# Kernel tuning notes

Measured on AMD Instinct MI355X. Metric: run time of the kernel, lower is better.

Reference implementation:

```python
import jax, jax.numpy as jnp
import numpy as np

VOCAB, EMB, H, NL = 50257, 1024, 2048, 2


def _lstm_cell(x, h, c, Wih, Whh, bih, bhh):
    # x: [1, in], h/c: [1, H]; PyTorch gate order i, f, g, o
    gates = x @ Wih.T + bih + h @ Whh.T + bhh  # [1, 4H]
    i, f, g, o = jnp.split(gates, 4, axis=-1)
    c2 = jax.nn.sigmoid(f) * c + jax.nn.sigmoid(i) * jnp.tanh(g)
    h2 = jax.nn.sigmoid(o) * jnp.tanh(c2)
    return h2, c2


def setup_inputs() -> dict:
    key = jax.random.key(0)
    ks = jax.random.split(key, 12)
    s = 0.02  # keep gate pre-activations in a sane range
    return {
        "input_ids": jax.random.randint(ks[0], (1,), 0, VOCAB, dtype=jnp.int64),
        "h0": jax.random.normal(ks[1], (2 * NL, 1, H), jnp.float32) * 0.1,
        "c0": jax.random.normal(ks[2], (2 * NL, 1, H), jnp.float32) * 0.1,
        "emb": jax.random.normal(ks[3], (VOCAB, EMB), jnp.float32),
        "W_ih_l0": jax.random.normal(ks[4], (2, 4 * H, EMB), jnp.float32) * s,
        "W_hh_l0": jax.random.normal(ks[5], (2, 4 * H, H), jnp.float32) * s,
        "b_ih_l0": jax.random.normal(ks[6], (2, 4 * H), jnp.float32) * s,
        "b_hh_l0": jax.random.normal(ks[7], (2, 4 * H), jnp.float32) * s,
        "W_ih_l1": jax.random.normal(ks[8], (2, 4 * H, 2 * H), jnp.float32) * s,
        "W_hh_l1": jax.random.normal(ks[9], (2, 4 * H, H), jnp.float32) * s,
        "b_ih_l1": jax.random.normal(ks[10], (2, 4 * H), jnp.float32) * s,
        "b_hh_l1": jax.random.normal(ks[11], (2, 4 * H), jnp.float32) * s,
    }


def reference(input_ids, h0, c0, emb, W_ih_l0, W_hh_l0, b_ih_l0, b_hh_l0,
              W_ih_l1, W_hh_l1, b_ih_l1, b_hh_l1):
    # embedded = embedding(input).view(1, 1, -1) -> seq_len=1, batch=1
    x = emb[input_ids]  # [1, EMB]
    layers = [(W_ih_l0, W_hh_l0, b_ih_l0, b_hh_l0),
              (W_ih_l1, W_hh_l1, b_ih_l1, b_hh_l1)]
    h_out, c_out = [], []
    for l, (Wih, Whh, bih, bhh) in enumerate(layers):
        # seq_len == 1: fwd and bwd directions both see the single timestep
        hf, cf = _lstm_cell(x, h0[2 * l], c0[2 * l], Wih[0], Whh[0], bih[0], bhh[0])
        hb, cb = _lstm_cell(x, h0[2 * l + 1], c0[2 * l + 1], Wih[1], Whh[1], bih[1], bhh[1])
        h_out += [hf, hb]
        c_out += [cf, cb]
        x = jnp.concatenate([hf, hb], axis=-1)  # [1, 2H] input to next layer
    output = x[None]  # [1, 1, 2H] (seq, batch, 2*hidden)
    h_n = jnp.stack(h_out, axis=0)  # [2*NL, 1, H]
    c_n = jnp.stack(c_out, axis=0)
    return output, h_n, c_n
```

## Files before the change

### kernel.cpp

```cpp
#include <hip/hip_runtime.h>


#define HID 2048
#define G4H 8192

__device__ __forceinline__ float wave_reduce_sum(float v) {
    #pragma unroll
    for (int off = 32; off > 0; off >>= 1)
        v += __shfl_down(v, off, 64);
    return v;
}

__global__ __launch_bounds__(256) void phase1_kernel(
    const int*   __restrict__ tok,
    const float* __restrict__ emb,
    const float* __restrict__ Wih0,
    const float* __restrict__ Whh0,
    const float* __restrict__ bih0,
    const float* __restrict__ bhh0,
    const float* __restrict__ Whh1,
    const float* __restrict__ bih1,
    const float* __restrict__ bhh1,
    const float* __restrict__ h0,
    float* __restrict__ gates0,
    float* __restrict__ part1)
{
    const int wave = (int)((blockIdx.x * blockDim.x + threadIdx.x) >> 6);
    const int lane = (int)(threadIdx.x & 63);

    if (wave < 2 * G4H) {
        const int dir = wave >> 13;
        const int r   = wave & (G4H - 1);
        const float*  x   = emb + (size_t)tok[0] * 1024;
        const float4* wih = (const float4*)(Wih0 + ((size_t)dir * G4H + r) * 1024);
        const float4* whh = (const float4*)(Whh0 + ((size_t)dir * G4H + r) * HID);
        const float4* xv  = (const float4*)x;
        const float4* hv  = (const float4*)(h0 + (size_t)dir * HID);

        float acc = 0.f;
        #pragma unroll
        for (int i = 0; i < 1024 / 4 / 64; ++i) {
            float4 w = wih[lane + i * 64], b = xv[lane + i * 64];
            acc += w.x * b.x + w.y * b.y + w.z * b.z + w.w * b.w;
        }
        #pragma unroll
        for (int i = 0; i < HID / 4 / 64; ++i) {
            float4 w = whh[lane + i * 64], b = hv[lane + i * 64];
            acc += w.x * b.x + w.y * b.y + w.z * b.z + w.w * b.w;
        }
        acc = wave_reduce_sum(acc);
        if (lane == 0) {
            int row = dir * G4H + r;
            gates0[row] = acc + bih0[row] + bhh0[row];
        }
    } else {
        const int w2  = wave - 2 * G4H;
        const int dir = w2 >> 13;
        const int r   = w2 & (G4H - 1);
        const float4* whh = (const float4*)(Whh1 + ((size_t)dir * G4H + r) * HID);
        const float4* hv  = (const float4*)(h0 + (size_t)(2 + dir) * HID);

        float acc = 0.f;
        #pragma unroll
        for (int i = 0; i < HID / 4 / 64; ++i) {
            float4 w = whh[lane + i * 64], b = hv[lane + i * 64];
            acc += w.x * b.x + w.y * b.y + w.z * b.z + w.w * b.w;
        }
        acc = wave_reduce_sum(acc);
        if (lane == 0) {
            int row = dir * G4H + r;
            part1[row] = acc + bih1[row] + bhh1[row];
        }
    }
}

__global__ __launch_bounds__(256) void phase2_kernel(
    const float* __restrict__ x1,
    const float* __restrict__ Wih1,
    const float* __restrict__ part1,
    float* __restrict__ gates)
{
    const int wave = (int)((blockIdx.x * blockDim.x + threadIdx.x) >> 6);
    const int lane = (int)(threadIdx.x & 63);
    const int dir  = wave >> 13;
    const int r    = wave & (G4H - 1);

    const float4* wih = (const float4*)(Wih1 + ((size_t)dir * G4H + r) * 4096);
    const float4* xv  = (const float4*)x1;

    float acc = 0.f;
    #pragma unroll
    for (int i = 0; i < 4096 / 4 / 64; ++i) {
        float4 w = wih[lane + i * 64], b = xv[lane + i * 64];
        acc += w.x * b.x + w.y * b.y + w.z * b.z + w.w * b.w;
    }
    acc = wave_reduce_sum(acc);
    if (lane == 0) {
        int row = dir * G4H + r;
        gates[row] = acc + part1[row];
    }
}

__device__ __forceinline__ float sigmoidf_(float v) {
    return 1.f / (1.f + expf(-v));
}

__global__ __launch_bounds__(256) void cell_kernel(
    const float* __restrict__ gates,
    const float* __restrict__ c0,
    int lo,
    float* __restrict__ hn,
    float* __restrict__ cn,
    float* __restrict__ xout)
{
    const int idx = (int)(blockIdx.x * blockDim.x + threadIdx.x);
    const int d = idx >> 11;
    const int j = idx & (HID - 1);

    const float* g = gates + d * G4H;
    float gi = g[j];
    float gf = g[HID + j];
    float gg = g[2 * HID + j];
    float go = g[3 * HID + j];

    float c_prev = c0[(size_t)(lo + d) * HID + j];
    float c2 = sigmoidf_(gf) * c_prev + sigmoidf_(gi) * tanhf(gg);
    float h2 = sigmoidf_(go) * tanhf(c2);

    hn[(size_t)(lo + d) * HID + j] = h2;
    cn[(size_t)(lo + d) * HID + j] = c2;
    xout[(size_t)d * HID + j] = h2;
}

extern "C" void kernel_launch(void* const* d_in, const int* in_sizes, int n_in,
                              void* d_out, int out_size, void* d_ws, size_t ws_size,
                              hipStream_t stream) {
    const int*   ids  = (const int*)  d_in[0];
    const float* h0   = (const float*)d_in[1];
    const float* c0   = (const float*)d_in[2];
    const float* emb  = (const float*)d_in[3];
    const float* Wih0 = (const float*)d_in[4];
    const float* Whh0 = (const float*)d_in[5];
    const float* bih0 = (const float*)d_in[6];
    const float* bhh0 = (const float*)d_in[7];
    const float* Wih1 = (const float*)d_in[8];
    const float* Whh1 = (const float*)d_in[9];
    const float* bih1 = (const float*)d_in[10];
    const float* bhh1 = (const float*)d_in[11];

    float* out    = (float*)d_out;
    float* gates  = (float*)d_ws;
    float* part1  = gates + 2 * G4H;
    float* x1     = part1 + 2 * G4H;

    phase1_kernel<<<8192, 256, 0, stream>>>(ids, emb, Wih0, Whh0, bih0, bhh0,
                                            Whh1, bih1, bhh1, h0, gates, part1);
    cell_kernel<<<16, 256, 0, stream>>>(gates, c0, 0, out + 4096, out + 12288, x1);
    phase2_kernel<<<4096, 256, 0, stream>>>(x1, Wih1, part1, gates);
    cell_kernel<<<16, 256, 0, stream>>>(gates, c0, 2, out + 4096, out + 12288, out);
}
```

Before: 106.3 us.

## Fuse layer-0 cell and layer-1 cell into the layer-1 input GEMV kernel

Drops the two small cell kernels. Each block of the layer-1 kernel now recomputes the full layer-0 LSTM cell into shared memory, and each wave computes all four gate rows for one hidden unit so it can apply the layer-1 cell directly. Launches go from four to two, and the gate round-trip through global memory is removed. The cost is that every one of 1024 blocks repeats the layer-0 cell work (16 elements per thread, including transcendentals), and each wave now streams four weight rows, so fewer waves are in flight.

After: 116.9 us. 10.0% more time.

```diff
diff --git a/kernel.cpp b/kernel.cpp
--- a/kernel.cpp
+++ b/kernel.cpp
@@ -10,8 +10,9 @@
         v += __shfl_down(v, off, 64);
     return v;
 }
+__device__ __forceinline__ float sigmoidf_(float v) { return 1.f / (1.f + expf(-v)); }
 
-__global__ __launch_bounds__(256) void phase1_kernel(
+__global__ __launch_bounds__(256) void k1_gates0_part1(
     const int*   __restrict__ tok,
     const float* __restrict__ emb,
     const float* __restrict__ Wih0,
@@ -74,62 +75,68 @@
     }
 }
 
-__global__ __launch_bounds__(256) void phase2_kernel(
-    const float* __restrict__ x1,
+__global__ __launch_bounds__(256) void k2_layer1(
+    const float* __restrict__ gates0,
+    const float* __restrict__ part1,
     const float* __restrict__ Wih1,
-    const float* __restrict__ part1,
-    float* __restrict__ gates)
+    const float* __restrict__ c0,
+    float* __restrict__ out)
 {
+    __shared__ float x1[2 * HID];
+
+    #pragma unroll
+    for (int k = 0; k < 16; ++k) {
+        const int idx = k * 256 + (int)threadIdx.x;
+        const int dir = idx >> 11;
+        const int j   = idx & (HID - 1);
+        const float* g = gates0 + dir * G4H;
+        float gi = g[j];
+        float gf = g[HID + j];
+        float gg = g[2 * HID + j];
+        float go = g[3 * HID + j];
+        float cp = c0[(size_t)dir * HID + j];
+        float c2 = sigmoidf_(gf) * cp + sigmoidf_(gi) * tanhf(gg);
+        float h2 = sigmoidf_(go) * tanhf(c2);
+        x1[idx] = h2;
+        if (blockIdx.x == 0) {
+            out[4096  + (size_t)dir * HID + j] = h2;
+            out[12288 + (size_t)dir * HID + j] = c2;
+        }
+    }
+    __syncthreads();
+
     const int wave = (int)((blockIdx.x * blockDim.x + threadIdx.x) >> 6);
     const int lane = (int)(threadIdx.x & 63);
-    const int dir  = wave >> 13;
-    const int r    = wave & (G4H - 1);
+    const int dir  = wave >> 11;
+    const int j    = wave & (HID - 1);
 
-    const float4* wih = (const float4*)(Wih1 + ((size_t)dir * G4H + r) * 4096);
-    const float4* xv  = (const float4*)x1;
+    const float4* xv = (const float4*)x1;
+    float acc[4] = {0.f, 0.f, 0.f, 0.f};
+    #pragma unroll
+    for (int g = 0; g < 4; ++g) {
+        const float4* wih = (const float4*)(Wih1 + ((size_t)dir * G4H + g * HID + j) * 4096);
+        #pragma unroll 4
+        for (int i = 0; i < 4096 / 4 / 64; ++i) {
+            float4 w = wih[lane + i * 64], b = xv[lane + i * 64];
+            acc[g] += w.x * b.x + w.y * b.y + w.z * b.z + w.w * b.w;
+        }
+    }
+    #pragma unroll
+    for (int g = 0; g < 4; ++g) acc[g] = wave_reduce_sum(acc[g]);
 
-    float acc = 0.f;
-    #pragma unroll
-    for (int i = 0; i < 4096 / 4 / 64; ++i) {
-        float4 w = wih[lane + i * 64], b = xv[lane + i * 64];
-        acc += w.x * b.x + w.y * b.y + w.z * b.z + w.w * b.w;
+    if (lane == 0) {
+        const int rb = dir * G4H + j;
+        float gi = acc[0] + part1[rb];
+        float gf = acc[1] + part1[rb + HID];
+        float gg = acc[2] + part1[rb + 2 * HID];
+        float go = acc[3] + part1[rb + 3 * HID];
+        float cp = c0[(size_t)(2 + dir) * HID + j];
+        float c2 = sigmoidf_(gf) * cp + sigmoidf_(gi) * tanhf(gg);
+        float h2 = sigmoidf_(go) * tanhf(c2);
+        out[4096  + (size_t)(2 + dir) * HID + j] = h2;
+        out[12288 + (size_t)(2 + dir) * HID + j] = c2;
+        out[(size_t)dir * HID + j] = h2;
     }
-    acc = wave_reduce_sum(acc);
-    if (lane == 0) {
-        int row = dir * G4H + r;
-        gates[row] = acc + part1[row];
-    }
-}
-
-__device__ __forceinline__ float sigmoidf_(float v) {
-    return 1.f / (1.f + expf(-v));
-}
-
-__global__ __launch_bounds__(256) void cell_kernel(
-    const float* __restrict__ gates,
-    const float* __restrict__ c0,
-    int lo,
-    float* __restrict__ hn,
-    float* __restrict__ cn,
-    float* __restrict__ xout)
-{
-    const int idx = (int)(blockIdx.x * blockDim.x + threadIdx.x);
-    const int d = idx >> 11;
-    const int j = idx & (HID - 1);
-
-    const float* g = gates + d * G4H;
-    float gi = g[j];
-    float gf = g[HID + j];
-    float gg = g[2 * HID + j];
-    float go = g[3 * HID + j];
-
-    float c_prev = c0[(size_t)(lo + d) * HID + j];
-    float c2 = sigmoidf_(gf) * c_prev + sigmoidf_(gi) * tanhf(gg);
-    float h2 = sigmoidf_(go) * tanhf(c2);
-
-    hn[(size_t)(lo + d) * HID + j] = h2;
-    cn[(size_t)(lo + d) * HID + j] = c2;
-    xout[(size_t)d * HID + j] = h2;
 }
 
 extern "C" void kernel_launch(void* const* d_in, const int* in_sizes, int n_in,
@@ -149,13 +156,10 @@
     const float* bhh1 = (const float*)d_in[11];
 
     float* out    = (float*)d_out;
-    float* gates  = (float*)d_ws;
-    float* part1  = gates + 2 * G4H;
-    float* x1     = part1 + 2 * G4H;
+    float* gates0 = (float*)d_ws;
+    float* part1  = gates0 + 2 * G4H;
 
-    phase1_kernel<<<8192, 256, 0, stream>>>(ids, emb, Wih0, Whh0, bih0, bhh0,
-                                            Whh1, bih1, bhh1, h0, gates, part1);
-    cell_kernel<<<16, 256, 0, stream>>>(gates, c0, 0, out + 4096, out + 12288, x1);
-    phase2_kernel<<<4096, 256, 0, stream>>>(x1, Wih1, part1, gates);
-    cell_kernel<<<16, 256, 0, stream>>>(gates, c0, 2, out + 4096, out + 12288, out);
+    k1_gates0_part1<<<8192, 256, 0, stream>>>(ids, emb, Wih0, Whh0, bih0, bhh0,
+                                              Whh1, bih1, bhh1, h0, gates0, part1);
+    k2_layer1<<<1024, 256, 0, stream>>>(gates0, part1, Wih1, c0, out);
 }
```
